# Performance work log

Measured on AMD Instinct MI355X. Metric: run time of the kernel, lower is better.

The kernel has to match this reference:

```python
import jax, jax.numpy as jnp
import numpy as np


def setup_inputs() -> dict:
    key = jax.random.key(0)
    k1, k2 = jax.random.split(key)
    x = jax.random.normal(k1, (32, 128, 128, 128), dtype=jnp.float32)
    conv_w = jax.random.normal(k2, (1, 2, 7, 7), dtype=jnp.float32) * 0.1
    return {"x": x, "conv_w": conv_w}


def reference(x, conv_w):
    # x: [B, C, H, W]; conv_w: [1, 2, 7, 7]
    max_out = jnp.max(x, axis=1, keepdims=True)   # [B,1,H,W]
    avg_out = jnp.mean(x, axis=1, keepdims=True)  # [B,1,H,W]
    stacked = jnp.concatenate([avg_out, max_out], axis=1)  # [B,2,H,W]
    attn = jax.lax.conv_general_dilated(
        stacked, conv_w,
        window_strides=(1, 1), padding=((3, 3), (3, 3)),
        dimension_numbers=("NCHW", "OIHW", "NCHW"),
    )  # [B,1,H,W]
    return x * jax.nn.sigmoid(attn)
```

## Files before the change

### kernel.cpp

```cpp
#include <hip/hip_runtime.h>

#define BB 32
#define CC 128
#define HH 128
#define WW 128
#define HWSZ (HH * WW)
#define CHW (CC * HWSZ)
#define S4 (HWSZ / 4)
#define RPB 8
#define HALO 14

typedef float vfloat4 __attribute__((ext_vector_type(4)));

__device__ __forceinline__ vfloat4 fmax4(vfloat4 a, vfloat4 b) {
    vfloat4 r;
    r.x = fmaxf(a.x, b.x);
    r.y = fmaxf(a.y, b.y);
    r.z = fmaxf(a.z, b.z);
    r.w = fmaxf(a.w, b.w);
    return r;
}

__global__ __launch_bounds__(256, 2) void sa_onepass(
    const float* __restrict__ x, const float* __restrict__ cw,
    float* __restrict__ out) {
    __shared__ float m_lds[2][HALO][WW];
    __shared__ float sig_lds[RPB][WW];
    __shared__ float wsh[2 * 49];

    const int tid = threadIdx.x;
    const int wg  = blockIdx.x;
    const int xcd = wg & 7;
    const int lin = wg >> 3;
    const int b   = xcd * 4 + (lin >> 4);
    const int hb  = lin & 15;
    const int h0  = hb * RPB;

    if (tid < 98) wsh[tid] = cw[tid];

    const int r0 = tid >> 5;
    const int w4 = tid & 31;
    const float* xb = x + (size_t)b * CHW;

    const bool actB = (r0 < HALO - 8);
    const int gh_a = h0 - 3 + r0;
    const int gh_b = h0 - 3 + r0 + 8;
    const bool okA = (gh_a >= 0) && (gh_a < HH);
    const bool okB = actB && (gh_b < HH);
    const int cha = gh_a < 0 ? 0 : (gh_a > HH - 1 ? HH - 1 : gh_a);
    const int chb = gh_b > HH - 1 ? HH - 1 : gh_b;

    const vfloat4* pA = (const vfloat4*)(xb + cha * WW) + w4;
    const vfloat4* pB = (const vfloat4*)(xb + chb * WW) + w4;

    vfloat4 sumA, mxA;
    {
        vfloat4 v = pA[0];
        sumA = v; mxA = v;
    }
    #pragma unroll 8
    for (int c = 1; c < CC; ++c) {
        vfloat4 v = pA[(size_t)c * S4];
        sumA += v;
        mxA = fmax4(mxA, v);
    }
    vfloat4 sumB = {0.f, 0.f, 0.f, 0.f}, mxB = sumB;
    if (actB) {
        vfloat4 v = pB[0];
        sumB = v; mxB = v;
        #pragma unroll 8
        for (int c = 1; c < CC; ++c) {
            vfloat4 t = pB[(size_t)c * S4];
            sumB += t;
            mxB = fmax4(mxB, t);
        }
    }

    const float invC = 1.0f / (float)CC;
    {
        vfloat4 avgA = sumA * invC;
        if (!okA) { avgA = (vfloat4){0,0,0,0}; mxA = (vfloat4){0,0,0,0}; }
        *(vfloat4*)&m_lds[0][r0][w4 * 4] = avgA;
        *(vfloat4*)&m_lds[1][r0][w4 * 4] = mxA;
        if (actB) {
            vfloat4 avgB = sumB * invC;
            if (!okB) { avgB = (vfloat4){0,0,0,0}; mxB = (vfloat4){0,0,0,0}; }
            *(vfloat4*)&m_lds[0][r0 + 8][w4 * 4] = avgB;
            *(vfloat4*)&m_lds[1][r0 + 8][w4 * 4] = mxB;
        }
    }
    __syncthreads();

    {
        const int q = tid >> 7;
        const int w = tid & 127;
        float attn[4] = {0.f, 0.f, 0.f, 0.f};
        #pragma unroll
        for (int ic = 0; ic < 2; ++ic) {
            #pragma unroll
            for (int L = 0; L < 10; ++L) {
                const float* row = &m_lds[ic][q * 4 + L][0];
                #pragma unroll
                for (int kw = 0; kw < 7; ++kw) {
                    int wi = w - 3 + kw;
                    float v = (wi >= 0 && wi < WW) ? row[wi] : 0.0f;
                    #pragma unroll
                    for (int j = 0; j < 4; ++j) {
                        const int kh = L - j;
                        if (kh >= 0 && kh <= 6)
                            attn[j] = fmaf(v, wsh[ic * 49 + kh * 7 + kw], attn[j]);
                    }
                }
            }
        }
        #pragma unroll
        for (int j = 0; j < 4; ++j)
            sig_lds[q * 4 + j][w] = 1.0f / (1.0f + __expf(-attn[j]));
    }
    __syncthreads();

    {
        const int wv = tid >> 6;
        const int ln = tid & 63;
        vfloat4 sgv[4];
        #pragma unroll
        for (int j = 0; j < 4; ++j) {
            int idx = ln + 64 * j;
            sgv[j] = *(const vfloat4*)&sig_lds[idx >> 5][(idx & 31) * 4];
        }
        const size_t slab_off = (size_t)h0 * WW;
        #pragma unroll 2
        for (int k = 31; k >= 0; --k) {
            const int c = wv + 4 * k;
            const vfloat4* ps = (const vfloat4*)(xb + (size_t)c * HWSZ + slab_off);
            vfloat4* po = (vfloat4*)(out + (size_t)b * CHW + (size_t)c * HWSZ + slab_off);
            vfloat4 v0 = ps[ln];
            vfloat4 v1 = ps[ln + 64];
            vfloat4 v2 = ps[ln + 128];
            vfloat4 v3 = ps[ln + 192];
            __builtin_nontemporal_store(v0 * sgv[0], po + ln);
            __builtin_nontemporal_store(v1 * sgv[1], po + ln + 64);
            __builtin_nontemporal_store(v2 * sgv[2], po + ln + 128);
            __builtin_nontemporal_store(v3 * sgv[3], po + ln + 192);
        }
    }
}

extern "C" void kernel_launch(void* const* d_in, const int* in_sizes, int n_in,
                              void* d_out, int out_size, void* d_ws, size_t ws_size,
                              hipStream_t stream) {
    const float* x  = (const float*)d_in[0];
    const float* cw = (const float*)d_in[1];
    float* out = (float*)d_out;

    sa_onepass<<<BB * (HH / RPB), 256, 0, stream>>>(x, cw, out);
}
```

Before: 140.9 us.

## Split into channel-reduce and conv-multiply kernels to remove halo recomputation

Splits the fused kernel into two. The first reduces each row over channels exactly once into a workspace map, and the second loads the halo rows of those maps into LDS, runs the 7x7 conv and sigmoid, then scales x. This removes the redundant channel reductions of the 6 halo rows per 8-row block, which were about 75% extra reads of x. In exchange it adds a second launch, a small workspace round-trip and a global barrier between the phases. The fused kernel is kept as a fallback for when the workspace is too small.

```diff
diff --git a/kernel.cpp b/kernel.cpp
--- a/kernel.cpp
+++ b/kernel.cpp
@@ -21,9 +21,33 @@
     return r;
 }
 
-__global__ __launch_bounds__(256, 2) void sa_onepass(
-    const float* __restrict__ x, const float* __restrict__ cw,
-    float* __restrict__ out) {
+
+__global__ __launch_bounds__(256) void k1_reduce(
+    const float* __restrict__ x, float* __restrict__ maps) {
+    const int tid = threadIdx.x;
+    const int wg  = blockIdx.x;
+    const int b   = wg >> 4;
+    const int hb  = wg & 15;
+    const int gh  = hb * RPB + (tid >> 5);
+    const int w4  = tid & 31;
+
+    const vfloat4* p = (const vfloat4*)(x + (size_t)b * CHW + gh * WW) + w4;
+    vfloat4 v = p[0];
+    vfloat4 sum = v, mx = v;
+    #pragma unroll 8
+    for (int c = 1; c < CC; ++c) {
+        vfloat4 t = p[(size_t)c * S4];
+        sum += t;
+        mx = fmax4(mx, t);
+    }
+    vfloat4 avg = sum * (1.0f / (float)CC);
+    *((vfloat4*)(maps + ((size_t)b * 2 + 0) * HWSZ + gh * WW) + w4) = avg;
+    *((vfloat4*)(maps + ((size_t)b * 2 + 1) * HWSZ + gh * WW) + w4) = mx;
+}
+
+__global__ __launch_bounds__(256, 2) void k2_conv_mul(
+    const float* __restrict__ x, const float* __restrict__ maps,
+    const float* __restrict__ cw, float* __restrict__ out) {
     __shared__ float m_lds[2][HALO][WW];
     __shared__ float sig_lds[RPB][WW];
     __shared__ float wsh[2 * 49];
@@ -38,56 +62,16 @@
 
     if (tid < 98) wsh[tid] = cw[tid];
 
-    const int r0 = tid >> 5;
-    const int w4 = tid & 31;
-    const float* xb = x + (size_t)b * CHW;
-
-    const bool actB = (r0 < HALO - 8);
-    const int gh_a = h0 - 3 + r0;
-    const int gh_b = h0 - 3 + r0 + 8;
-    const bool okA = (gh_a >= 0) && (gh_a < HH);
-    const bool okB = actB && (gh_b < HH);
-    const int cha = gh_a < 0 ? 0 : (gh_a > HH - 1 ? HH - 1 : gh_a);
-    const int chb = gh_b > HH - 1 ? HH - 1 : gh_b;
-
-    const vfloat4* pA = (const vfloat4*)(xb + cha * WW) + w4;
-    const vfloat4* pB = (const vfloat4*)(xb + chb * WW) + w4;
-
-    vfloat4 sumA, mxA;
-    {
-        vfloat4 v = pA[0];
-        sumA = v; mxA = v;
-    }
-    #pragma unroll 8
-    for (int c = 1; c < CC; ++c) {
-        vfloat4 v = pA[(size_t)c * S4];
-        sumA += v;
-        mxA = fmax4(mxA, v);
-    }
-    vfloat4 sumB = {0.f, 0.f, 0.f, 0.f}, mxB = sumB;
-    if (actB) {
-        vfloat4 v = pB[0];
-        sumB = v; mxB = v;
-        #pragma unroll 8
-        for (int c = 1; c < CC; ++c) {
-            vfloat4 t = pB[(size_t)c * S4];
-            sumB += t;
-            mxB = fmax4(mxB, t);
-        }
-    }
-
-    const float invC = 1.0f / (float)CC;
-    {
-        vfloat4 avgA = sumA * invC;
-        if (!okA) { avgA = (vfloat4){0,0,0,0}; mxA = (vfloat4){0,0,0,0}; }
-        *(vfloat4*)&m_lds[0][r0][w4 * 4] = avgA;
-        *(vfloat4*)&m_lds[1][r0][w4 * 4] = mxA;
-        if (actB) {
-            vfloat4 avgB = sumB * invC;
-            if (!okB) { avgB = (vfloat4){0,0,0,0}; mxB = (vfloat4){0,0,0,0}; }
-            *(vfloat4*)&m_lds[0][r0 + 8][w4 * 4] = avgB;
-            *(vfloat4*)&m_lds[1][r0 + 8][w4 * 4] = mxB;
-        }
+    for (int i = tid; i < 2 * HALO * 32; i += 256) {
+        const int ic = i / (HALO * 32);
+        const int rem = i - ic * (HALO * 32);
+        const int rr = rem >> 5;
+        const int w4 = rem & 31;
+        const int gh = h0 - 3 + rr;
+        vfloat4 v = {0.f, 0.f, 0.f, 0.f};
+        if (gh >= 0 && gh < HH)
+            v = *((const vfloat4*)(maps + ((size_t)b * 2 + ic) * HWSZ + gh * WW) + w4);
+        *(vfloat4*)&m_lds[ic][rr][w4 * 4] = v;
     }
     __syncthreads();
 
@@ -120,6 +104,7 @@
     __syncthreads();
 
     {
+        const float* xb = x + (size_t)b * CHW;
         const int wv = tid >> 6;
         const int ln = tid & 63;
         vfloat4 sgv[4];
@@ -146,6 +131,131 @@
     }
 }
 
+__global__ __launch_bounds__(256, 2) void sa_onepass(
+    const float* __restrict__ x, const float* __restrict__ cw,
+    float* __restrict__ out) {
+    __shared__ float m_lds[2][HALO][WW];
+    __shared__ float sig_lds[RPB][WW];
+    __shared__ float wsh[2 * 49];
+
+    const int tid = threadIdx.x;
+    const int wg  = blockIdx.x;
+    const int xcd = wg & 7;
+    const int lin = wg >> 3;
+    const int b   = xcd * 4 + (lin >> 4);
+    const int hb  = lin & 15;
+    const int h0  = hb * RPB;
+
+    if (tid < 98) wsh[tid] = cw[tid];
+
+    const int r0 = tid >> 5;
+    const int w4 = tid & 31;
+    const float* xb = x + (size_t)b * CHW;
+
+    const bool actB = (r0 < HALO - 8);
+    const int gh_a = h0 - 3 + r0;
+    const int gh_b = h0 - 3 + r0 + 8;
+    const bool okA = (gh_a >= 0) && (gh_a < HH);
+    const bool okB = actB && (gh_b < HH);
+    const int cha = gh_a < 0 ? 0 : (gh_a > HH - 1 ? HH - 1 : gh_a);
+    const int chb = gh_b > HH - 1 ? HH - 1 : gh_b;
+
+    const vfloat4* pA = (const vfloat4*)(xb + cha * WW) + w4;
+    const vfloat4* pB = (const vfloat4*)(xb + chb * WW) + w4;
+
+    vfloat4 sumA, mxA;
+    {
+        vfloat4 v = pA[0];
+        sumA = v; mxA = v;
+    }
+    #pragma unroll 8
+    for (int c = 1; c < CC; ++c) {
+        vfloat4 v = pA[(size_t)c * S4];
+        sumA += v;
+        mxA = fmax4(mxA, v);
+    }
+    vfloat4 sumB = {0.f, 0.f, 0.f, 0.f}, mxB = sumB;
+    if (actB) {
+        vfloat4 v = pB[0];
+        sumB = v; mxB = v;
+        #pragma unroll 8
+        for (int c = 1; c < CC; ++c) {
+            vfloat4 t = pB[(size_t)c * S4];
+            sumB += t;
+            mxB = fmax4(mxB, t);
+        }
+    }
+
+    const float invC = 1.0f / (float)CC;
+    {
+        vfloat4 avgA = sumA * invC;
+        if (!okA) { avgA = (vfloat4){0,0,0,0}; mxA = (vfloat4){0,0,0,0}; }
+        *(vfloat4*)&m_lds[0][r0][w4 * 4] = avgA;
+        *(vfloat4*)&m_lds[1][r0][w4 * 4] = mxA;
+        if (actB) {
+            vfloat4 avgB = sumB * invC;
+            if (!okB) { avgB = (vfloat4){0,0,0,0}; mxB = (vfloat4){0,0,0,0}; }
+            *(vfloat4*)&m_lds[0][r0 + 8][w4 * 4] = avgB;
+            *(vfloat4*)&m_lds[1][r0 + 8][w4 * 4] = mxB;
+        }
+    }
+    __syncthreads();
+
+    {
+        const int q = tid >> 7;
+        const int w = tid & 127;
+        float attn[4] = {0.f, 0.f, 0.f, 0.f};
+        #pragma unroll
+        for (int ic = 0; ic < 2; ++ic) {
+            #pragma unroll
+            for (int L = 0; L < 10; ++L) {
+                const float* row = &m_lds[ic][q * 4 + L][0];
+                #pragma unroll
+                for (int kw = 0; kw < 7; ++kw) {
+                    int wi = w - 3 + kw;
+                    float v = (wi >= 0 && wi < WW) ? row[wi] : 0.0f;
+                    #pragma unroll
+                    for (int j = 0; j < 4; ++j) {
+                        const int kh = L - j;
+                        if (kh >= 0 && kh <= 6)
+                            attn[j] = fmaf(v, wsh[ic * 49 + kh * 7 + kw], attn[j]);
+                    }
+                }
+            }
+        }
+        #pragma unroll
+        for (int j = 0; j < 4; ++j)
+            sig_lds[q * 4 + j][w] = 1.0f / (1.0f + __expf(-attn[j]));
+    }
+    __syncthreads();
+
+    {
+        const int wv = tid >> 6;
+        const int ln = tid & 63;
+        vfloat4 sgv[4];
+        #pragma unroll
+        for (int j = 0; j < 4; ++j) {
+            int idx = ln + 64 * j;
+            sgv[j] = *(const vfloat4*)&sig_lds[idx >> 5][(idx & 31) * 4];
+        }
+        const size_t slab_off = (size_t)h0 * WW;
+        #pragma unroll 2
+        for (int k = 31; k >= 0; --k) {
+            const int c = wv + 4 * k;
+            const vfloat4* ps = (const vfloat4*)(xb + (size_t)c * HWSZ + slab_off);
+            vfloat4* po = (vfloat4*)(out + (size_t)b * CHW + (size_t)c * HWSZ + slab_off);
+            vfloat4 v0 = ps[ln];
+            vfloat4 v1 = ps[ln + 64];
+            vfloat4 v2 = ps[ln + 128];
+            vfloat4 v3 = ps[ln + 192];
+            __builtin_nontemporal_store(v0 * sgv[0], po + ln);
+            __builtin_nontemporal_store(v1 * sgv[1], po + ln + 64);
+            __builtin_nontemporal_store(v2 * sgv[2], po + ln + 128);
+            __builtin_nontemporal_store(v3 * sgv[3], po + ln + 192);
+        }
+    }
+}
+
 extern "C" void kernel_launch(void* const* d_in, const int* in_sizes, int n_in,
                               void* d_out, int out_size, void* d_ws, size_t ws_size,
                               hipStream_t stream) {
@@ -153,5 +263,12 @@
     const float* cw = (const float*)d_in[1];
     float* out = (float*)d_out;
 
-    sa_onepass<<<BB * (HH / RPB), 256, 0, stream>>>(x, cw, out);
-}
+    const size_t maps_bytes = (size_t)BB * 2 * HWSZ * sizeof(float);
+    if (ws_size >= maps_bytes) {
+        float* maps = (float*)d_ws;
+        k1_reduce<<<BB * (HH / RPB), 256, 0, stream>>>(x, maps);
+        k2_conv_mul<<<BB * (HH / RPB), 256, 0, stream>>>(x, maps, cw, out);
+    } else {
+        sa_onepass<<<BB * (HH / RPB), 256, 0, stream>>>(x, cw, out);
+    }
+}
```

Measured after the change: 133.0 us (median of 2 runs). 5.6% less time.
